# Optimization experiments

Measured on AMD Instinct MI355X. Metric: run time of the kernel, lower is better.

Reference implementation:

```python
import jax, jax.numpy as jnp
import numpy as np

DIM = 1024
H = 16
N_OSC = 1
DT = 0.1
NUM_STEPS = 5
CAUSAL = False


def setup_inputs() -> dict:
    key = jax.random.key(0)
    ks = jax.random.split(key, 6)
    B, T, D = 2, 2048, DIM
    x = jax.random.normal(ks[0], (B, T, D), dtype=jnp.float32)
    # nn.Linear weights, stored (out, in) like torch; y = x @ W.T
    s = 1.0 / np.sqrt(D)
    Wq = jax.random.uniform(ks[1], (D, D), jnp.float32, -s, s)
    Wk = jax.random.uniform(ks[2], (D, D), jnp.float32, -s, s)
    Wv = jax.random.uniform(ks[3], (D, D), jnp.float32, -s, s)
    Wo = jax.random.uniform(ks[4], (D, D), jnp.float32, -s, s)
    omega = jax.random.normal(ks[5], (H, N_OSC), dtype=jnp.float32) * 0.1
    return {"x": x, "Wq": Wq, "Wk": Wk, "Wv": Wv, "Wo": Wo, "omega": omega}


def reference(x, Wq, Wk, Wv, Wo, omega):
    B, T, D = x.shape
    dk = D // H
    scale = 1.0 / np.sqrt(dk).astype(np.float32)
    two_pi = jnp.float32(2.0 * np.pi)

    def heads(W):
        # (B,T,D) -> (B,H,T,dk)
        return (x @ W.T).reshape(B, T, H, dk).transpose(0, 2, 1, 3)

    q = heads(Wq)
    k = heads(Wk)
    v = heads(Wv)

    # coupling J_ij = softmax_j(q_i . k_j / sqrt(dk)) -> (B,H,T,T)
    logits = jnp.einsum("bhid,bhjd->bhij", q, k) * scale
    if CAUSAL:
        mask = jnp.triu(jnp.ones((T, T), dtype=bool), k=1)
        logits = jnp.where(mask[None, None], -jnp.inf, logits)
    J = jax.nn.softmax(logits, axis=-1)

    # initial phases from v: atan2(sum of first N_OSC dims, sum of next N_OSC dims)
    phases = jnp.arctan2(
        v[..., :N_OSC].sum(-1), v[..., N_OSC:2 * N_OSC].sum(-1) + 1e-8
    )  # (B,H,T)

    # omega broadcast to (B,H,T): (H,1)->(1,H,1,1)->(B,H,T,1)->squeeze
    om = jnp.broadcast_to(omega[None, :, None, :], (B, H, T, N_OSC))[..., 0]

    def step(ph, _):
        # diff[...,i,j] = phi_i - phi_j
        diff = ph[..., :, None] - ph[..., None, :]
        coupling = (J * jnp.sin(diff)).sum(-1)
        ph = (ph + DT * (om + coupling)) % two_pi
        return ph, None

    phases, _ = jax.lax.scan(step, phases, None, length=NUM_STEPS)

    v_mod = v * jnp.cos(phases)[..., None]  # (B,H,T,dk)
    out = v_mod.transpose(0, 2, 1, 3).reshape(B, T, D) @ Wo.T
    return x + out
```

## Files before the change

### kernel.cpp

```cpp
#include <hip/hip_runtime.h>
#include <hip/hip_bf16.h>

#define B_    2
#define T_    2048
#define D_    1024
#define H_    16
#define DK_   64
#define BH_   (B_*H_)
#define M_    (B_*T_)
#define NSTEP 5
#define DT_   0.1f
#define TWO_PI_F 6.28318530717958647692f
#define JROWS 8

typedef __attribute__((ext_vector_type(8))) short s16x8;
typedef __attribute__((ext_vector_type(4))) float f32x4;
typedef __attribute__((ext_vector_type(2))) float f32x2;

__device__ __forceinline__ unsigned short f2bf(float f) {
  unsigned int u = __float_as_uint(f);
  u += 0x7FFFu + ((u >> 16) & 1u);
  return (unsigned short)(u >> 16);
}

__device__ __forceinline__ void gload_lds16(const void* g, void* l) {
  __builtin_amdgcn_global_load_lds(
      (const __attribute__((address_space(1))) unsigned int*)g,
      (__attribute__((address_space(3))) unsigned int*)l, 16, 0, 0);
}

__device__ __forceinline__ void conv8(const float* in, unsigned short* out, int i) {
  const float4* p = (const float4*)in + (size_t)i*2;
  float4 a = p[0], b = p[1];
  s16x8 o;
  o[0]=(short)f2bf(a.x); o[1]=(short)f2bf(a.y); o[2]=(short)f2bf(a.z); o[3]=(short)f2bf(a.w);
  o[4]=(short)f2bf(b.x); o[5]=(short)f2bf(b.y); o[6]=(short)f2bf(b.z); o[7]=(short)f2bf(b.w);
  *(s16x8*)(out + (size_t)i*8) = o;
}

__global__ void conv_all(const float* __restrict__ x,
                         const float* __restrict__ wq, const float* __restrict__ wk,
                         const float* __restrict__ wv, const float* __restrict__ wo,
                         unsigned short* __restrict__ xb,
                         unsigned short* __restrict__ oq, unsigned short* __restrict__ ok,
                         unsigned short* __restrict__ ov, unsigned short* __restrict__ oo)
{
  int bid = blockIdx.x;
  if (bid < 2048) {
    conv8(x, xb, bid*256 + threadIdx.x);
  } else {
    int r = bid - 2048;
    int z = r >> 9, lb = r & 511;
    const float* in = (z==0)?wq:(z==1)?wk:(z==2)?wv:wo;
    unsigned short* out = (z==0)?oq:(z==1)?ok:(z==2)?ov:oo;
    conv8(in, out, lb*256 + threadIdx.x);
  }
}

template<int BM, int MODE>
__device__ __forceinline__ void gemm_body(const unsigned short* __restrict__ A,
    const unsigned short* __restrict__ W, void* __restrict__ outp,
    const float* __restrict__ res, float scale, int m0, int n0)
{
  constexpr int MF = BM/32;
  __shared__ unsigned short lA[BM*64];
  __shared__ unsigned short lB[128*64];
  const int t = threadIdx.x, wv = t >> 6, lane = t & 63;
  const int wm = wv >> 1, wn = wv & 1;
  const int lr = lane & 15, kg = lane >> 4;
  const int lrow = lane >> 3, sch = (lane & 7) ^ lrow;

  f32x4 acc[MF][4];
#pragma unroll
  for (int i = 0; i < MF; ++i)
#pragma unroll
    for (int j = 0; j < 4; ++j) { acc[i][j][0]=0.f; acc[i][j][1]=0.f; acc[i][j][2]=0.f; acc[i][j][3]=0.f; }

  for (int kt = 0; kt < 1024; kt += 64) {
#pragma unroll
    for (int ii = 0; ii < BM/32; ++ii) {
      const int inst = wv*(BM/32) + ii;
      const int row  = inst*8 + lrow;
      gload_lds16(A + (size_t)(m0+row)*1024 + kt + sch*8, lA + inst*512);
    }
#pragma unroll
    for (int ii = 0; ii < 4; ++ii) {
      const int inst = wv*4 + ii;
      const int row  = inst*8 + lrow;
      gload_lds16(W + (size_t)(n0+row)*1024 + kt + sch*8, lB + inst*512);
    }
    __syncthreads();

    s16x8 a0[MF], a1[MF], b0[4], b1[4];
#pragma unroll
    for (int mf = 0; mf < MF; ++mf) {
      int row = wm*(BM/2) + mf*16 + lr, s7 = row & 7;
      a0[mf] = *(const s16x8*)(lA + row*64 + ((kg^s7)*8));
      a1[mf] = *(const s16x8*)(lA + row*64 + (((kg+4)^s7)*8));
    }
#pragma unroll
    for (int nf = 0; nf < 4; ++nf) {
      int row = wn*64 + nf*16 + lr, s7 = row & 7;
      b0[nf] = *(const s16x8*)(lB + row*64 + ((kg^s7)*8));
      b1[nf] = *(const s16x8*)(lB + row*64 + (((kg+4)^s7)*8));
    }
#pragma unroll
    for (int mf = 0; mf < MF; ++mf)
#pragma unroll
      for (int nf = 0; nf < 4; ++nf) {
        acc[mf][nf] = __builtin_amdgcn_mfma_f32_16x16x32_bf16(a0[mf], b0[nf], acc[mf][nf], 0,0,0);
        acc[mf][nf] = __builtin_amdgcn_mfma_f32_16x16x32_bf16(a1[mf], b1[nf], acc[mf][nf], 0,0,0);
      }
    __syncthreads();
  }

#pragma unroll
  for (int mf = 0; mf < MF; ++mf)
#pragma unroll
    for (int nf = 0; nf < 4; ++nf)
#pragma unroll
      for (int r = 0; r < 4; ++r) {
        int grow = m0 + wm*(BM/2) + mf*16 + kg*4 + r;
        int gcol = n0 + wn*64 + nf*16 + lr;
        size_t o = (size_t)grow*1024 + gcol;
        float v = acc[mf][nf][r];
        if (MODE == 0) ((unsigned short*)outp)[o] = f2bf(v*scale);
        else           ((float*)outp)[o] = v + res[o];
      }
}

__global__ __launch_bounds__(256)
void gemm_qkv(const unsigned short* __restrict__ xb,
              const unsigned short* __restrict__ wq, const unsigned short* __restrict__ wk,
              const unsigned short* __restrict__ wv_,
              unsigned short* __restrict__ Qb, unsigned short* __restrict__ Kb,
              unsigned short* __restrict__ Vb)
{
  const int z = blockIdx.z;
  const unsigned short* W = (z==0)?wq:((z==1)?wk:wv_);
  unsigned short* O = (z==0)?Qb:((z==1)?Kb:Vb);
  const float scale = (z==0) ? 0.125f : 1.0f;
  gemm_body<128,0>(xb, W, O, nullptr, scale, blockIdx.x*128, blockIdx.y*128);
}

__global__ __launch_bounds__(256)
void gemm_o(const unsigned short* __restrict__ Ab, const unsigned short* __restrict__ wo,
            float* __restrict__ out, const float* __restrict__ x)
{
  gemm_body<64,2>(Ab, wo, out, x, 1.0f, blockIdx.x*64, blockIdx.y*128);
}

__global__ __launch_bounds__(256)
void v01_kernel(const float* __restrict__ x, const float* __restrict__ Wv,
                float* __restrict__ V01)
{
  const int t = threadIdx.x;
  const int colid = t & 31;
  const int row = blockIdx.x*8 + (t >> 5);
  const int wcol = (colid >> 1)*DK_ + (colid & 1);
  const float4* xr = (const float4*)(x  + (size_t)row*1024);
  const float4* wr = (const float4*)(Wv + (size_t)wcol*1024);
  float acc = 0.f;
  for (int k = 0; k < 256; ++k) {
    float4 a = xr[k], b = wr[k];
    acc += a.x*b.x + a.y*b.y + a.z*b.z + a.w*b.w;
  }
  V01[(size_t)row*32 + colid] = acc;
}

__global__ void phase_init2(const float* __restrict__ V01, float* __restrict__ ph,
                            float* __restrict__ cw, float* __restrict__ sw)
{
  int idx = blockIdx.x*256 + threadIdx.x;
  int tt = idx & (T_-1);
  int bh = idx >> 11;
  int b = bh >> 4, h = bh & 15;
  float a = V01[((size_t)(b*T_ + tt))*32 + h*2 + 0];
  float c = V01[((size_t)(b*T_ + tt))*32 + h*2 + 1] + 1e-8f;
  ph[idx] = atan2f(a, c);
  float r = fmaxf(sqrtf(a*a + c*c), 1e-30f);
  cw[idx] = c / r;
  sw[idx] = a / r;
}

__global__ __launch_bounds__(256)
void build_cse2(const unsigned short* __restrict__ Qb, const unsigned short* __restrict__ Kb,
                unsigned char* __restrict__ J,
                const float* __restrict__ cr, const float* __restrict__ sr,
                float* __restrict__ parts)
{
  __shared__ unsigned short lK[2][128*64];
  const int ib = blockIdx.x, jc = blockIdx.y, bh = blockIdx.z;
  const int b = bh >> 4, h = bh & 15;
  const int t = threadIdx.x, wv = t >> 6, lane = t & 63;
  const int wj = wv >> 1, wi = wv & 1;
  const int lr = lane & 15, kg = lane >> 4;
  const int lrow = lane >> 3, sch = (lane & 7) ^ lrow;
  const int i0 = ib*128;

  const unsigned short* Kbase = Kb + (size_t)b*T_*D_ + h*DK_;
  const unsigned short* Qbase = Qb + (size_t)b*T_*D_ + h*DK_;
  const float* crow = cr + (size_t)bh*T_;
  const float* srow = sr + (size_t)bh*T_;

#pragma unroll
  for (int ii = 0; ii < 4; ++ii) {
    const int inst = wv*4 + ii;
    const int row  = inst*8 + lrow;
    gload_lds16(Qbase + (size_t)(i0 + row)*D_ + sch*8, &lK[0][inst*512]);
  }
  __syncthreads();

  s16x8 bq0[4], bq1[4];
#pragma unroll
  for (int ti = 0; ti < 4; ++ti) {
    int row = wi*64 + ti*16 + lr, s7 = row & 7;
    bq0[ti] = *(const s16x8*)(&lK[0][row*64 + ((kg^s7)*8)]);
    bq1[ti] = *(const s16x8*)(&lK[0][row*64 + (((kg+4)^s7)*8)]);
  }
  __syncthreads();

#pragma unroll
  for (int ii = 0; ii < 4; ++ii) {
    const int inst = wv*4 + ii;
    const int row  = inst*8 + lrow;
    gload_lds16(Kbase + (size_t)(jc*1024 + row)*D_ + sch*8, &lK[0][inst*512]);
  }
  __syncthreads();

  float Cp[4] = {0.f,0.f,0.f,0.f};
  float Sp[4] = {0.f,0.f,0.f,0.f};
  float Ep[4] = {0.f,0.f,0.f,0.f};

  for (int tt = 0; tt < 8; ++tt) {
    const int cur = tt & 1;
    if (tt < 7) {
#pragma unroll
      for (int ii = 0; ii < 4; ++ii) {
        const int inst = wv*4 + ii;
        const int row  = inst*8 + lrow;
        gload_lds16(Kbase + (size_t)(jc*1024 + (tt+1)*128 + row)*D_ + sch*8,
                    &lK[cur^1][inst*512]);
      }
    }

    const int jb0 = jc*1024 + tt*128 + wj*64;
    s16x8 ak0[4], ak1[4];
    float4 cj[4], sj[4];
#pragma unroll
    for (int s = 0; s < 4; ++s) {
      int row = wj*64 + s*16 + lr, s7 = row & 7;
      ak0[s] = *(const s16x8*)(&lK[cur][row*64 + ((kg^s7)*8)]);
      ak1[s] = *(const s16x8*)(&lK[cur][row*64 + (((kg+4)^s7)*8)]);
      cj[s] = *(const float4*)(crow + jb0 + s*16 + kg*4);
      sj[s] = *(const float4*)(srow + jb0 + s*16 + kg*4);
    }

#pragma unroll
    for (int ti = 0; ti < 4; ++ti) {
      unsigned char* Jrow = J + ((size_t)(bh*T_ + i0 + wi*64 + ti*16 + lr))*T_ + jb0 + kg*4;
#pragma unroll
      for (int s = 0; s < 4; ++s) {
        f32x4 dd; dd[0]=0.f; dd[1]=0.f; dd[2]=0.f; dd[3]=0.f;
        dd = __builtin_amdgcn_mfma_f32_16x16x32_bf16(ak0[s], bq0[ti], dd, 0, 0, 0);
        dd = __builtin_amdgcn_mfma_f32_16x16x32_bf16(ak1[s], bq1[ti], dd, 0, 0, 0);
        float e0 = __expf(dd[0]), e1 = __expf(dd[1]);
        float e2 = __expf(dd[2]), e3 = __expf(dd[3]);
        unsigned int p = 0;
        p = __builtin_amdgcn_cvt_pk_fp8_f32(e0, e1, p, false);
        p = __builtin_amdgcn_cvt_pk_fp8_f32(e2, e3, p, true);
        *(unsigned int*)(Jrow + s*16) = p;
        Cp[ti] += e0*cj[s].x + e1*cj[s].y + e2*cj[s].z + e3*cj[s].w;
        Sp[ti] += e0*sj[s].x + e1*sj[s].y + e2*sj[s].z + e3*sj[s].w;
        Ep[ti] += (e0 + e1) + (e2 + e3);
      }
    }
    asm volatile("s_waitcnt lgkmcnt(0)" ::: "memory");
    __builtin_amdgcn_sched_barrier(0);
    __builtin_amdgcn_s_barrier();
  }

#pragma unroll
  for (int m = 16; m < 64; m <<= 1)
#pragma unroll
    for (int ti = 0; ti < 4; ++ti) {
      Cp[ti] += __shfl_xor(Cp[ti], m);
      Sp[ti] += __shfl_xor(Sp[ti], m);
      Ep[ti] += __shfl_xor(Ep[ti], m);
    }
  if (kg == 0) {
    const size_t N = (size_t)BH_*T_;
    const int chunk = jc*2 + wj;
#pragma unroll
    for (int ti = 0; ti < 4; ++ti) {
      size_t row = (size_t)bh*T_ + i0 + wi*64 + ti*16 + lr;
      parts[(0*4 + chunk)*N + row] = Cp[ti];
      parts[(1*4 + chunk)*N + row] = Sp[ti];
      parts[(2*4 + chunk)*N + row] = Ep[ti];
    }
  }
}

__global__ void finalize1(const float* __restrict__ parts,
                          const float* __restrict__ cr, const float* __restrict__ sr,
                          float* __restrict__ cw, float* __restrict__ sw,
                          float* __restrict__ ph, const float* __restrict__ omega)
{
  int idx = blockIdx.x*256 + threadIdx.x;
  const size_t N = (size_t)BH_*T_;
  float C = parts[0*N+idx] + parts[1*N+idx] + parts[2*N+idx] + parts[3*N+idx];
  float S = parts[4*N+idx] + parts[5*N+idx] + parts[6*N+idx] + parts[7*N+idx];
  float E = parts[8*N+idx] + parts[9*N+idx] + parts[10*N+idx] + parts[11*N+idx];
  int bh = idx >> 11;
  float si = sr[idx], ci = cr[idx];
  float coupling = (si*C - ci*S) / E;
  float pn = ph[idx] + DT_*(omega[bh & 15] + coupling);
  pn = fmodf(pn, TWO_PI_F);
  if (pn < 0.f) pn += TWO_PI_F;
  ph[idx] = pn;
  cw[idx] = __cosf(pn);
  sw[idx] = __sinf(pn);
}

__global__ __launch_bounds__(256)
void j_step2(const unsigned char* __restrict__ J,
             const float* __restrict__ cr, const float* __restrict__ sr,
             float* __restrict__ cw, float* __restrict__ sw,
             float* __restrict__ ph, const float* __restrict__ omega)
{
  const int wv = threadIdx.x >> 6, lane = threadIdx.x & 63;
  const int r0 = (blockIdx.x*4 + wv)*JROWS;
  const int bh = r0 >> 11;
  const float4* c4 = (const float4*)(cr + (size_t)bh*T_);
  const float4* s4 = (const float4*)(sr + (size_t)bh*T_);

  f32x2 C2[JROWS], S2[JROWS], E2[JROWS];
#pragma unroll
  for (int r = 0; r < JROWS; ++r) {
    C2[r][0]=0.f; C2[r][1]=0.f; S2[r][0]=0.f; S2[r][1]=0.f; E2[r][0]=0.f; E2[r][1]=0.f;
  }

#pragma unroll
  for (int k = 0; k < 2; ++k) {
    int idx = k*64 + lane;
    f32x2 clo[4], chi[4], slo[4], shi[4];
#pragma unroll
    for (int q = 0; q < 4; ++q) {
      float4 cv = c4[idx*4+q], sv = s4[idx*4+q];
      clo[q][0]=cv.x; clo[q][1]=cv.y; chi[q][0]=cv.z; chi[q][1]=cv.w;
      slo[q][0]=sv.x; slo[q][1]=sv.y; shi[q][0]=sv.z; shi[q][1]=sv.w;
    }
#pragma unroll
    for (int row = 0; row < JROWS; ++row) {
      uint4 jv = *(const uint4*)(J + (size_t)(r0+row)*T_ + (size_t)idx*16);
#pragma unroll
      for (int q = 0; q < 4; ++q) {
        unsigned int wq_ = (q==0)?jv.x:(q==1)?jv.y:(q==2)?jv.z:jv.w;
        f32x2 lo = __builtin_amdgcn_cvt_pk_f32_fp8(wq_, false);
        f32x2 hi = __builtin_amdgcn_cvt_pk_f32_fp8(wq_, true);
        C2[row] += lo*clo[q] + hi*chi[q];
        S2[row] += lo*slo[q] + hi*shi[q];
        E2[row] += lo + hi;
      }
    }
  }

  float C[JROWS], S[JROWS], E[JROWS];
#pragma unroll
  for (int r = 0; r < JROWS; ++r) { C[r]=C2[r][0]+C2[r][1]; S[r]=S2[r][0]+S2[r][1]; E[r]=E2[r][0]+E2[r][1]; }

#pragma unroll
  for (int m = 1; m < 64; m <<= 1) {
#pragma unroll
    for (int row = 0; row < JROWS; ++row) {
      C[row] += __shfl_xor(C[row], m);
      S[row] += __shfl_xor(S[row], m);
      E[row] += __shfl_xor(E[row], m);
    }
  }

  if (lane < JROWS) {
    float Cc = C[0], Ss = S[0], Ee = E[0];
#pragma unroll
    for (int r = 1; r < JROWS; ++r)
      if (lane == r) { Cc = C[r]; Ss = S[r]; Ee = E[r]; }
    int pidx = r0 + lane;
    float si = sr[pidx], ci = cr[pidx];
    float om = omega[bh & 15];
    float coupling = (si*Cc - ci*Ss) / Ee;
    float pn = ph[pidx] + DT_*(om + coupling);
    pn = fmodf(pn, TWO_PI_F);
    if (pn < 0.f) pn += TWO_PI_F;
    ph[pidx] = pn;
    cw[pidx] = __cosf(pn);
    sw[pidx] = __sinf(pn);
  }
}

__global__ void vmod2(unsigned short* __restrict__ V, const float* __restrict__ cfin)
{
  int idx = blockIdx.x*256 + threadIdx.x;
  int row = idx >> 7;
  int g = idx & 127;
  int h = g >> 3;
  int b = row >> 11, tt = row & 2047;
  float c = cfin[((size_t)(b*H_ + h))*T_ + tt];
  s16x8 v = *(s16x8*)(V + (size_t)idx*8);
  s16x8 o;
#pragma unroll
  for (int e = 0; e < 8; ++e) {
    float f = __uint_as_float(((unsigned int)(unsigned short)v[e]) << 16);
    o[e] = (short)f2bf(f * c);
  }
  *(s16x8*)(V + (size_t)idx*8) = o;
}

extern "C" void kernel_launch(void* const* d_in, const int* in_sizes, int n_in,
                              void* d_out, int out_size, void* d_ws, size_t ws_size,
                              hipStream_t stream)
{
  const float* x     = (const float*)d_in[0];
  const float* Wq    = (const float*)d_in[1];
  const float* Wk    = (const float*)d_in[2];
  const float* Wv    = (const float*)d_in[3];
  const float* Wo    = (const float*)d_in[4];
  const float* omega = (const float*)d_in[5];
  float* out = (float*)d_out;

  char* w = (char*)d_ws;
  unsigned short* Qb  = (unsigned short*)w; w += (size_t)M_*D_*2;
  unsigned short* Kb  = (unsigned short*)w; w += (size_t)M_*D_*2;
  unsigned short* Vb  = (unsigned short*)w; w += (size_t)M_*D_*2;
  unsigned short* wob = (unsigned short*)w; w += (size_t)D_*D_*2;
  float* ph   = (float*)w; w += (size_t)BH_*T_*4;
  float* csb[2]; float* snb[2];
  csb[0] = (float*)w; w += (size_t)BH_*T_*4;
  snb[0] = (float*)w; w += (size_t)BH_*T_*4;
  csb[1] = (float*)w; w += (size_t)BH_*T_*4;
  snb[1] = (float*)w; w += (size_t)BH_*T_*4;
  float* V01   = (float*)w; w += (size_t)M_*32*4;
  float* parts = (float*)w; w += (size_t)3*4*BH_*T_*4;
  unsigned char* J = (unsigned char*)w;
  unsigned short* xb  = (unsigned short*)J;
  unsigned short* wqb = (unsigned short*)(J + (size_t)M_*D_*2);
  unsigned short* wkb = wqb + (size_t)D_*D_;
  unsigned short* wvb = wkb + (size_t)D_*D_;

  conv_all<<<4096, 256, 0, stream>>>(x, Wq, Wk, Wv, Wo, xb, wqb, wkb, wvb, wob);

  gemm_qkv<<<dim3(M_/128, D_/128, 3), 256, 0, stream>>>(xb, wqb, wkb, wvb, Qb, Kb, Vb);

  v01_kernel<<<M_/8, 256, 0, stream>>>(x, Wv, V01);
  phase_init2<<<BH_*T_/256, 256, 0, stream>>>(V01, ph, csb[0], snb[0]);

  build_cse2<<<dim3(T_/128, 2, BH_), 256, 0, stream>>>(Qb, Kb, J, csb[0], snb[0], parts);
  finalize1<<<BH_*T_/256, 256, 0, stream>>>(parts, csb[0], snb[0], csb[1], snb[1], ph, omega);

  for (int s = 1; s < NSTEP; ++s)
    j_step2<<<BH_*T_/(4*JROWS), 256, 0, stream>>>(J, csb[s&1], snb[s&1],
                                                  csb[(s+1)&1], snb[(s+1)&1], ph, omega);

  vmod2<<<M_*D_/8/256, 256, 0, stream>>>(Vb, csb[NSTEP&1]);
  gemm_o<<<dim3(M_/64, D_/128), 256, 0, stream>>>(Vb, wob, out, x);
}
```

Measured before the change: 340.2 us.

## Tile J build as 128x128 blocks with LDS-staged coalesced fp8 stores

Replaces the build kernel, which streamed 1024 K columns per block with double-buffered K loads, by a 2D grid of 128x128 tiles that each load one K tile and one Q tile. The fp8 exp(logits) are staged in swizzled LDS and then written to global memory as 16-byte coalesced rows, replacing scattered 4-byte stores. Partial C/S/E sums are reduced across waves in LDS and written as 16 chunks, so finalize now sums 16 partials. A fallback skips the fused first step when the workspace is too small, in which case step 0 runs through j_step2 instead.

```diff
diff --git a/kernel.cpp b/kernel.cpp
--- a/kernel.cpp
+++ b/kernel.cpp
@@ -184,13 +184,18 @@
 }
 
 __global__ __launch_bounds__(256)
-void build_cse2(const unsigned short* __restrict__ Qb, const unsigned short* __restrict__ Kb,
-                unsigned char* __restrict__ J,
-                const float* __restrict__ cr, const float* __restrict__ sr,
-                float* __restrict__ parts)
-{
-  __shared__ unsigned short lK[2][128*64];
-  const int ib = blockIdx.x, jc = blockIdx.y, bh = blockIdx.z;
+void build_t(const unsigned short* __restrict__ Qb, const unsigned short* __restrict__ Kb,
+             unsigned char* __restrict__ J,
+             const float* __restrict__ cr, const float* __restrict__ sr,
+             float* __restrict__ parts)
+{
+  __shared__ unsigned char lds[32768 + 3072];
+  unsigned short* lK = (unsigned short*)lds;
+  unsigned short* lQ = (unsigned short*)(lds + 16384);
+  unsigned char*  lJ = lds;
+  float* lRed = (float*)(lds + 32768);
+
+  const int ib = blockIdx.x, jb = blockIdx.y, bh = blockIdx.z;
   const int b = bh >> 4, h = bh & 15;
   const int t = threadIdx.x, wv = t >> 6, lane = t & 63;
   const int wj = wv >> 1, wi = wv & 1;
@@ -200,86 +205,62 @@
 
   const unsigned short* Kbase = Kb + (size_t)b*T_*D_ + h*DK_;
   const unsigned short* Qbase = Qb + (size_t)b*T_*D_ + h*DK_;
-  const float* crow = cr + (size_t)bh*T_;
-  const float* srow = sr + (size_t)bh*T_;
 
 #pragma unroll
   for (int ii = 0; ii < 4; ++ii) {
     const int inst = wv*4 + ii;
     const int row  = inst*8 + lrow;
-    gload_lds16(Qbase + (size_t)(i0 + row)*D_ + sch*8, &lK[0][inst*512]);
+    gload_lds16(Kbase + (size_t)(jb*128 + row)*D_ + sch*8, lK + inst*512);
+    gload_lds16(Qbase + (size_t)(i0 + row)*D_ + sch*8, lQ + inst*512);
   }
   __syncthreads();
 
-  s16x8 bq0[4], bq1[4];
+  s16x8 ak0[4], ak1[4], bq0[4], bq1[4];
+#pragma unroll
+  for (int s = 0; s < 4; ++s) {
+    int row = wj*64 + s*16 + lr, s7 = row & 7;
+    ak0[s] = *(const s16x8*)(lK + row*64 + ((kg^s7)*8));
+    ak1[s] = *(const s16x8*)(lK + row*64 + (((kg+4)^s7)*8));
+  }
 #pragma unroll
   for (int ti = 0; ti < 4; ++ti) {
     int row = wi*64 + ti*16 + lr, s7 = row & 7;
-    bq0[ti] = *(const s16x8*)(&lK[0][row*64 + ((kg^s7)*8)]);
-    bq1[ti] = *(const s16x8*)(&lK[0][row*64 + (((kg+4)^s7)*8)]);
-  }
-  __syncthreads();
-
-#pragma unroll
-  for (int ii = 0; ii < 4; ++ii) {
-    const int inst = wv*4 + ii;
-    const int row  = inst*8 + lrow;
-    gload_lds16(Kbase + (size_t)(jc*1024 + row)*D_ + sch*8, &lK[0][inst*512]);
+    bq0[ti] = *(const s16x8*)(lQ + row*64 + ((kg^s7)*8));
+    bq1[ti] = *(const s16x8*)(lQ + row*64 + (((kg+4)^s7)*8));
+  }
+  const float* crow = cr + (size_t)bh*T_;
+  const float* srow = sr + (size_t)bh*T_;
+  float4 cj[4], sj[4];
+#pragma unroll
+  for (int s = 0; s < 4; ++s) {
+    cj[s] = *(const float4*)(crow + jb*128 + wj*64 + s*16 + kg*4);
+    sj[s] = *(const float4*)(srow + jb*128 + wj*64 + s*16 + kg*4);
   }
   __syncthreads();
 
   float Cp[4] = {0.f,0.f,0.f,0.f};
   float Sp[4] = {0.f,0.f,0.f,0.f};
   float Ep[4] = {0.f,0.f,0.f,0.f};
-
-  for (int tt = 0; tt < 8; ++tt) {
-    const int cur = tt & 1;
-    if (tt < 7) {
-#pragma unroll
-      for (int ii = 0; ii < 4; ++ii) {
-        const int inst = wv*4 + ii;
-        const int row  = inst*8 + lrow;
-        gload_lds16(Kbase + (size_t)(jc*1024 + (tt+1)*128 + row)*D_ + sch*8,
-                    &lK[cur^1][inst*512]);
-      }
-    }
-
-    const int jb0 = jc*1024 + tt*128 + wj*64;
-    s16x8 ak0[4], ak1[4];
-    float4 cj[4], sj[4];
+#pragma unroll
+  for (int ti = 0; ti < 4; ++ti) {
+    const int row = wi*64 + ti*16 + lr;
+    const int rx = row & 7;
 #pragma unroll
     for (int s = 0; s < 4; ++s) {
-      int row = wj*64 + s*16 + lr, s7 = row & 7;
-      ak0[s] = *(const s16x8*)(&lK[cur][row*64 + ((kg^s7)*8)]);
-      ak1[s] = *(const s16x8*)(&lK[cur][row*64 + (((kg+4)^s7)*8)]);
-      cj[s] = *(const float4*)(crow + jb0 + s*16 + kg*4);
-      sj[s] = *(const float4*)(srow + jb0 + s*16 + kg*4);
-    }
-
-#pragma unroll
-    for (int ti = 0; ti < 4; ++ti) {
-      unsigned char* Jrow = J + ((size_t)(bh*T_ + i0 + wi*64 + ti*16 + lr))*T_ + jb0 + kg*4;
-#pragma unroll
-      for (int s = 0; s < 4; ++s) {
-        f32x4 dd; dd[0]=0.f; dd[1]=0.f; dd[2]=0.f; dd[3]=0.f;
-        dd = __builtin_amdgcn_mfma_f32_16x16x32_bf16(ak0[s], bq0[ti], dd, 0, 0, 0);
-        dd = __builtin_amdgcn_mfma_f32_16x16x32_bf16(ak1[s], bq1[ti], dd, 0, 0, 0);
-        float e0 = __expf(dd[0]), e1 = __expf(dd[1]);
-        float e2 = __expf(dd[2]), e3 = __expf(dd[3]);
-        unsigned int p = 0;
-        p = __builtin_amdgcn_cvt_pk_fp8_f32(e0, e1, p, false);
-        p = __builtin_amdgcn_cvt_pk_fp8_f32(e2, e3, p, true);
-        *(unsigned int*)(Jrow + s*16) = p;
-        Cp[ti] += e0*cj[s].x + e1*cj[s].y + e2*cj[s].z + e3*cj[s].w;
-        Sp[ti] += e0*sj[s].x + e1*sj[s].y + e2*sj[s].z + e3*sj[s].w;
-        Ep[ti] += (e0 + e1) + (e2 + e3);
-      }
-    }
-    asm volatile("s_waitcnt lgkmcnt(0)" ::: "memory");
-    __builtin_amdgcn_sched_barrier(0);
-    __builtin_amdgcn_s_barrier();
-  }
-
+      f32x4 dd; dd[0]=0.f; dd[1]=0.f; dd[2]=0.f; dd[3]=0.f;
+      dd = __builtin_amdgcn_mfma_f32_16x16x32_bf16(ak0[s], bq0[ti], dd, 0, 0, 0);
+      dd = __builtin_amdgcn_mfma_f32_16x16x32_bf16(ak1[s], bq1[ti], dd, 0, 0, 0);
+      float e0 = __expf(dd[0]), e1 = __expf(dd[1]);
+      float e2 = __expf(dd[2]), e3 = __expf(dd[3]);
+      unsigned int p = 0;
+      p = __builtin_amdgcn_cvt_pk_fp8_f32(e0, e1, p, false);
+      p = __builtin_amdgcn_cvt_pk_fp8_f32(e2, e3, p, true);
+      *(unsigned int*)(lJ + row*128 + (((wj*4 + s) ^ rx) << 4) + kg*4) = p;
+      Cp[ti] += e0*cj[s].x + e1*cj[s].y + e2*cj[s].z + e3*cj[s].w;
+      Sp[ti] += e0*sj[s].x + e1*sj[s].y + e2*sj[s].z + e3*sj[s].w;
+      Ep[ti] += (e0 + e1) + (e2 + e3);
+    }
+  }
 #pragma unroll
   for (int m = 16; m < 64; m <<= 1)
 #pragma unroll
@@ -289,15 +270,32 @@
       Ep[ti] += __shfl_xor(Ep[ti], m);
     }
   if (kg == 0) {
+#pragma unroll
+    for (int ti = 0; ti < 4; ++ti) {
+      int i = wi*64 + ti*16 + lr;
+      lRed[(wj*128 + i)*3 + 0] = Cp[ti];
+      lRed[(wj*128 + i)*3 + 1] = Sp[ti];
+      lRed[(wj*128 + i)*3 + 2] = Ep[ti];
+    }
+  }
+  __syncthreads();
+
+#pragma unroll
+  for (int it = 0; it < 4; ++it) {
+    int row = it*32 + (t >> 3);
+    int blk = t & 7;
+    uint4 v = *(const uint4*)(lJ + row*128 + (((blk ^ (row & 7)) << 4)));
+    *(uint4*)(J + ((size_t)(bh*T_ + i0 + row))*T_ + jb*128 + blk*16) = v;
+  }
+  if (parts != nullptr && t < 128) {
+    float C = lRed[t*3+0] + lRed[(128+t)*3+0];
+    float S = lRed[t*3+1] + lRed[(128+t)*3+1];
+    float E = lRed[t*3+2] + lRed[(128+t)*3+2];
     const size_t N = (size_t)BH_*T_;
-    const int chunk = jc*2 + wj;
-#pragma unroll
-    for (int ti = 0; ti < 4; ++ti) {
-      size_t row = (size_t)bh*T_ + i0 + wi*64 + ti*16 + lr;
-      parts[(0*4 + chunk)*N + row] = Cp[ti];
-      parts[(1*4 + chunk)*N + row] = Sp[ti];
-      parts[(2*4 + chunk)*N + row] = Ep[ti];
-    }
+    size_t rowg = (size_t)bh*T_ + i0 + t;
+    parts[(0*16 + jb)*N + rowg] = C;
+    parts[(1*16 + jb)*N + rowg] = S;
+    parts[(2*16 + jb)*N + rowg] = E;
   }
 }
 
@@ -308,9 +306,13 @@
 {
   int idx = blockIdx.x*256 + threadIdx.x;
   const size_t N = (size_t)BH_*T_;
-  float C = parts[0*N+idx] + parts[1*N+idx] + parts[2*N+idx] + parts[3*N+idx];
-  float S = parts[4*N+idx] + parts[5*N+idx] + parts[6*N+idx] + parts[7*N+idx];
-  float E = parts[8*N+idx] + parts[9*N+idx] + parts[10*N+idx] + parts[11*N+idx];
+  float C = 0.f, S = 0.f, E = 0.f;
+#pragma unroll
+  for (int c = 0; c < 16; ++c) {
+    C += parts[(0*16 + c)*N + idx];
+    S += parts[(1*16 + c)*N + idx];
+    E += parts[(2*16 + c)*N + idx];
+  }
   int bh = idx >> 11;
   float si = sr[idx], ci = cr[idx];
   float coupling = (si*C - ci*S) / E;
@@ -438,9 +440,10 @@
   snb[0] = (float*)w; w += (size_t)BH_*T_*4;
   csb[1] = (float*)w; w += (size_t)BH_*T_*4;
   snb[1] = (float*)w; w += (size_t)BH_*T_*4;
-  float* V01   = (float*)w; w += (size_t)M_*32*4;
-  float* parts = (float*)w; w += (size_t)3*4*BH_*T_*4;
-  unsigned char* J = (unsigned char*)w;
+  float* V01 = (float*)w; w += (size_t)M_*32*4;
+  unsigned char* J = (unsigned char*)w; w += (size_t)BH_*T_*T_;
+  float* parts = (float*)w; w += (size_t)3*16*BH_*T_*4;
+  const bool fuse = (ws_size >= (size_t)(w - (char*)d_ws));
   unsigned short* xb  = (unsigned short*)J;
   unsigned short* wqb = (unsigned short*)(J + (size_t)M_*D_*2);
   unsigned short* wkb = wqb + (size_t)D_*D_;
@@ -453,10 +456,17 @@
   v01_kernel<<<M_/8, 256, 0, stream>>>(x, Wv, V01);
   phase_init2<<<BH_*T_/256, 256, 0, stream>>>(V01, ph, csb[0], snb[0]);
 
-  build_cse2<<<dim3(T_/128, 2, BH_), 256, 0, stream>>>(Qb, Kb, J, csb[0], snb[0], parts);
-  finalize1<<<BH_*T_/256, 256, 0, stream>>>(parts, csb[0], snb[0], csb[1], snb[1], ph, omega);
-
-  for (int s = 1; s < NSTEP; ++s)
+  build_t<<<dim3(T_/128, T_/128, BH_), 256, 0, stream>>>(
+      Qb, Kb, J, csb[0], snb[0], fuse ? parts : nullptr);
+
+  int s0;
+  if (fuse) {
+    finalize1<<<BH_*T_/256, 256, 0, stream>>>(parts, csb[0], snb[0], csb[1], snb[1], ph, omega);
+    s0 = 1;
+  } else {
+    s0 = 0;
+  }
+  for (int s = s0; s < NSTEP; ++s)
     j_step2<<<BH_*T_/(4*JROWS), 256, 0, stream>>>(J, csb[s&1], snb[s&1],
                                                   csb[(s+1)&1], snb[(s+1)&1], ph, omega);
 
```

Result: faster. 308.6 us (-9.3%).
